# Kernel optimization log

Hardware: AMD Instinct MI355X
Metric: run time of the kernel (lower is better)

The kernel has to match this reference:

```python
import jax, jax.numpy as jnp
import numpy as np

B, TX, TY = 32, 64, 64
D, H, V = 512, 512, 32000
FORGET_BIAS = 1.0  # TF BasicLSTMCell default


def setup_inputs() -> dict:
    key = jax.random.key(0)
    ks = jax.random.split(key, 8)
    enc_ids = jax.random.randint(ks[0], (B, TX), 0, V, dtype=jnp.int32)
    dec_ids = jax.random.randint(ks[1], (B, TY), 0, V, dtype=jnp.int32)
    len_enc = jax.random.randint(ks[2], (B,), 1, TX + 1, dtype=jnp.int32)
    len_dec = jax.random.randint(ks[3], (B,), 1, TY + 1, dtype=jnp.int32)
    E = jax.random.normal(ks[4], (V, D), dtype=jnp.float32) * 0.05
    enc_W = jax.random.normal(ks[5], (D + H, 4 * H), dtype=jnp.float32) * (1.0 / np.sqrt(D + H))
    dec_W = jax.random.normal(ks[6], (D + H, 4 * H), dtype=jnp.float32) * (1.0 / np.sqrt(D + H))
    proj_W = jax.random.normal(ks[7], (H, V), dtype=jnp.float32) * (1.0 / np.sqrt(H))
    return {
        'encoder_inputs': enc_ids, 'decoder_inputs': dec_ids,
        'length_encoder': len_enc, 'length_decoder': len_dec,
        'E': E, 'enc_W': enc_W, 'enc_b': jnp.zeros((4 * H,), jnp.float32),
        'dec_W': dec_W, 'dec_b': jnp.zeros((4 * H,), jnp.float32),
        'proj_W': proj_W,
    }


def _lstm_scan(x_seq, lengths, W, b, c0, h0):
    """Masked LSTM over x_seq [T,B,D]; mimics tf.nn.dynamic_rnn sequence_length
    semantics (state frozen past each example's length). Returns (c,h,hs)."""
    def step(carry, x):
        c, h, t = carry
        z = jnp.concatenate([x, h], axis=-1) @ W + b  # [B,4H]
        i, j, f, o = jnp.split(z, 4, axis=-1)  # TF BasicLSTMCell gate order
        c_new = c * jax.nn.sigmoid(f + FORGET_BIAS) + jax.nn.sigmoid(i) * jnp.tanh(j)
        h_new = jnp.tanh(c_new) * jax.nn.sigmoid(o)
        m = (t < lengths)[:, None]
        c = jnp.where(m, c_new, c)
        h_out = jnp.where(m, h_new, jnp.zeros_like(h_new))  # emitted output zeroed past length
        h = jnp.where(m, h_new, h)
        return (c, h, t + 1), h_out
    (c, h, _), hs = jax.lax.scan(step, (c0, h0, jnp.int32(0)), x_seq)
    return c, h, hs


def reference(encoder_inputs, decoder_inputs, length_encoder, length_decoder,
              E, enc_W, enc_b, dec_W, dec_b, proj_W):
    b = encoder_inputs.shape[0]
    # Encoder: embed + masked LSTM; keep final state.
    enc_x = E[encoder_inputs].transpose(1, 0, 2)  # [TX,B,D]
    z = jnp.zeros((b, enc_W.shape[1] // 4), jnp.float32)
    c, h, _ = _lstm_scan(enc_x, length_encoder, enc_W, enc_b, z, z)
    # Decoder: teacher-forced LSTM from encoder final state + vocab projection.
    dec_x = E[decoder_inputs].transpose(1, 0, 2)  # [TY,B,D]
    _, _, hs = _lstm_scan(dec_x, length_decoder, dec_W, dec_b, c, h)  # [TY,B,H]
    logits = jnp.einsum('tbh,hv->btv', hs, proj_W)  # [B,TY,V]
    # impute_finished=True zeroes outputs past each sequence length
    mask = (jnp.arange(logits.shape[1])[None, :] < length_decoder[:, None])[:, :, None]
    return jnp.where(mask, logits, 0.0)
```

## Files before the change

### kernel.cpp

```cpp
#include <hip/hip_runtime.h>

typedef unsigned short ushort_t;
typedef __attribute__((ext_vector_type(8))) short short8;
typedef __attribute__((ext_vector_type(4))) float f32x4;

__device__ __forceinline__ ushort_t f2bf(float x) {
  union { float f; unsigned int u; } v; v.f = x;
  unsigned int r = v.u + 0x7fffu + ((v.u >> 16) & 1u);
  return (ushort_t)(r >> 16);
}
__device__ __forceinline__ float bf2f(ushort_t h) {
  union { unsigned int u; float f; } v; v.u = ((unsigned int)h) << 16; return v.f;
}
__device__ __forceinline__ void splitbf(float x, ushort_t& hi, ushort_t& lo) {
  hi = f2bf(x);
  lo = f2bf(x - bf2f(hi));
}
__device__ __forceinline__ float sigm(float x) { return 1.f / (1.f + expf(-x)); }
__device__ __forceinline__ f32x4 mfma16(short8 a, short8 b, f32x4 c) {
  return __builtin_amdgcn_mfma_f32_16x16x32_bf16(a, b, c, 0, 0, 0);
}

#define BAR_NB 64
__device__ __forceinline__ void gridbar(int* __restrict__ flags, int bid,
                                        int bm, int tid, int bar) {
  asm volatile("s_waitcnt vmcnt(0)" ::: "memory");
  __syncthreads();
  if (tid == 0)
    __hip_atomic_store(&flags[bid * 32], bar, __ATOMIC_RELAXED,
                       __HIP_MEMORY_SCOPE_AGENT);
  if (tid < 32) {
    while (__hip_atomic_load(&flags[(2 * tid + bm) * 32], __ATOMIC_RELAXED,
                             __HIP_MEMORY_SCOPE_AGENT) < bar) {}
  }
  __syncthreads();
}

__global__ void __launch_bounds__(256) transpose_split(
    const float* __restrict__ src, int ld, int k0,
    ushort_t* __restrict__ hi, ushort_t* __restrict__ lo) {
  __shared__ float tile[64][65];
  const int n0 = blockIdx.x * 64, kb = blockIdx.y * 64;
  #pragma unroll
  for (int i = 0; i < 16; ++i) {
    int idx = i * 256 + threadIdx.x;
    int kk = idx >> 6, nn = idx & 63;
    tile[kk][nn] = src[(size_t)(k0 + kb + kk) * ld + n0 + nn];
  }
  __syncthreads();
  #pragma unroll
  for (int i = 0; i < 16; ++i) {
    int idx = i * 256 + threadIdx.x;
    int nn = idx >> 6, kk = idx & 63;
    float x = tile[kk][nn];
    ushort_t h, l; splitbf(x, h, l);
    size_t o = (size_t)(n0 + nn) * 512 + kb + kk;
    hi[o] = h; lo[o] = l;
  }
}

__global__ void __launch_bounds__(128) embed_split(
    const int* __restrict__ ids, const float* __restrict__ E,
    ushort_t* __restrict__ Ahi, ushort_t* __restrict__ Alo, int T) {
  const int m = blockIdx.x;
  const int b = m & 31, t = m >> 5;
  const int id = ids[b * T + t];
  float4 v = ((const float4*)(E + (size_t)id * 512))[threadIdx.x];
  ushort_t h0, l0, h1, l1, h2, l2, h3, l3;
  splitbf(v.x, h0, l0); splitbf(v.y, h1, l1);
  splitbf(v.z, h2, l2); splitbf(v.w, h3, l3);
  ushort4 hv = make_ushort4(h0, h1, h2, h3);
  ushort4 lv = make_ushort4(l0, l1, l2, l3);
  ((ushort4*)(Ahi + (size_t)m * 512))[threadIdx.x] = hv;
  ((ushort4*)(Alo + (size_t)m * 512))[threadIdx.x] = lv;
}

template <int MFAST>
__global__ void __launch_bounds__(256, 2) gemm_split_t(
    const ushort_t* __restrict__ Ahi, const ushort_t* __restrict__ Alo,
    const ushort_t* __restrict__ Bhi, const ushort_t* __restrict__ Blo,
    const float* __restrict__ bias, float* __restrict__ C, int M, int N) {
  __shared__ __align__(16) ushort_t lAh[128 * 64];
  __shared__ __align__(16) ushort_t lAl[128 * 64];
  __shared__ __align__(16) ushort_t lBh[128 * 64];
  __shared__ __align__(16) ushort_t lBl[128 * 64];
  const int tid = threadIdx.x;
  const int lane = tid & 63, w = tid >> 6;
  const int wm = (w >> 1) * 64, wn = (w & 1) * 64;
  const int lm = lane & 15, lq = lane >> 4;
  const int m0 = (MFAST ? blockIdx.x : blockIdx.y) * 128;
  const int n0 = (MFAST ? blockIdx.y : blockIdx.x) * 128;

  f32x4 acc[4][4];
  #pragma unroll
  for (int i = 0; i < 4; ++i)
    #pragma unroll
    for (int j = 0; j < 4; ++j)
      acc[i][j] = (f32x4){0.f, 0.f, 0.f, 0.f};

  for (int kc = 0; kc < 8; ++kc) {
    if (kc) __syncthreads();
    #pragma unroll
    for (int i = 0; i < 4; ++i) {
      int cid = i * 256 + tid;
      int r = cid >> 3, c = cid & 7;
      int cs = c ^ (r & 7);
      size_t goffA = (size_t)(m0 + r) * 512 + kc * 64 + c * 8;
      size_t goffB = (size_t)(n0 + r) * 512 + kc * 64 + c * 8;
      *(uint4*)&lAh[r * 64 + cs * 8] = *(const uint4*)(Ahi + goffA);
      *(uint4*)&lAl[r * 64 + cs * 8] = *(const uint4*)(Alo + goffA);
      *(uint4*)&lBh[r * 64 + cs * 8] = *(const uint4*)(Bhi + goffB);
      *(uint4*)&lBl[r * 64 + cs * 8] = *(const uint4*)(Blo + goffB);
    }
    __syncthreads();
    #pragma unroll
    for (int ks = 0; ks < 2; ++ks) {
      short8 ah[4], al[4], bh[4], bl[4];
      #pragma unroll
      for (int t = 0; t < 4; ++t) {
        int ra = wm + t * 16 + lm;
        int ca = (ks * 4 + lq) ^ (ra & 7);
        ah[t] = *(const short8*)&lAh[ra * 64 + ca * 8];
        al[t] = *(const short8*)&lAl[ra * 64 + ca * 8];
        int rb = wn + t * 16 + lm;
        int cb = (ks * 4 + lq) ^ (rb & 7);
        bh[t] = *(const short8*)&lBh[rb * 64 + cb * 8];
        bl[t] = *(const short8*)&lBl[rb * 64 + cb * 8];
      }
      #pragma unroll
      for (int mt = 0; mt < 4; ++mt)
        #pragma unroll
        for (int nt = 0; nt < 4; ++nt) {
          acc[mt][nt] = mfma16(ah[mt], bh[nt], acc[mt][nt]);
          acc[mt][nt] = mfma16(ah[mt], bl[nt], acc[mt][nt]);
          acc[mt][nt] = mfma16(al[mt], bh[nt], acc[mt][nt]);
        }
    }
  }
  #pragma unroll
  for (int nt = 0; nt < 4; ++nt) {
    int col = n0 + wn + nt * 16 + lm;
    float bv = bias ? bias[col] : 0.f;
    #pragma unroll
    for (int mt = 0; mt < 4; ++mt) {
      int rbase = m0 + wm + mt * 16 + lq * 4;
      #pragma unroll
      for (int r = 0; r < 4; ++r)
        C[(size_t)(rbase + r) * N + col] = acc[mt][nt][r] + bv;
    }
  }
}

__global__ void __launch_bounds__(256, 1) lstm_recurrence(
    const ushort_t* __restrict__ eWh_hi, const ushort_t* __restrict__ eWh_lo,
    const ushort_t* __restrict__ dWh_hi, const ushort_t* __restrict__ dWh_lo,
    const float* __restrict__ xz_enc, const float* __restrict__ xz_dec,
    const int* __restrict__ len_enc, const int* __restrict__ len_dec,
    ushort_t* __restrict__ hseq_hi, ushort_t* __restrict__ hseq_lo,
    ushort_t* __restrict__ hs_hi, ushort_t* __restrict__ hs_lo,
    int* __restrict__ flags) {
  const int tid = threadIdx.x;
  const int lane = tid & 63, g = tid >> 6;
  const int lm = lane & 15, lq = lane >> 4;
  const int bm = blockIdx.x & 1, jg = blockIdx.x >> 1;

  __shared__ float z_x[4][16][17];
  __shared__ float c_st[16][17], h_st[16][17];

  const int bl = tid >> 4, nn = tid & 15;
  const int bglob = bm * 16 + bl;
  const int hcol = jg * 16 + nn;

  c_st[bl][nn] = 0.f; h_st[bl][nn] = 0.f;
  __hip_atomic_store(&hseq_hi[bglob * 512 + hcol], (ushort_t)0,
                     __ATOMIC_RELAXED, __HIP_MEMORY_SCOPE_AGENT);
  __hip_atomic_store(&hseq_lo[bglob * 512 + hcol], (ushort_t)0,
                     __ATOMIC_RELAXED, __HIP_MEMORY_SCOPE_AGENT);
  const int lenE = len_enc[bglob], lenD = len_dec[bglob];

  short8 fbh[16], fbl[16];
  const size_t browoff = (size_t)(g * 512 + jg * 16 + lm) * 512 + lq * 8;
  #pragma unroll
  for (int ks = 0; ks < 16; ++ks) {
    fbh[ks] = *(const short8*)(eWh_hi + browoff + ks * 32);
    fbl[ks] = *(const short8*)(eWh_lo + browoff + ks * 32);
  }

  float pzi, pzj, pzf, pzo;
  {
    const size_t base = (size_t)bglob * 2048 + jg * 16 + nn;
    pzi = xz_enc[base];        pzj = xz_enc[base + 512];
    pzf = xz_enc[base + 1024]; pzo = xz_enc[base + 1536];
  }
  gridbar(flags, blockIdx.x, bm, tid, 1);

  const size_t arow = (size_t)(bm * 16 + lm) * 512 + lq * 8;

  #pragma unroll 1
  for (int s = 0; s < 128; ++s) {
    if (s == 64) {
      #pragma unroll
      for (int ks = 0; ks < 16; ++ks) {
        fbh[ks] = *(const short8*)(dWh_hi + browoff + ks * 32);
        fbl[ks] = *(const short8*)(dWh_lo + browoff + ks * 32);
      }
    }
    const ushort_t* hh = hseq_hi + (size_t)s * 16384;
    const ushort_t* hl = hseq_lo + (size_t)s * 16384;
    ushort_t* ohh = hseq_hi + (size_t)(s + 1) * 16384;
    ushort_t* ohl = hseq_lo + (size_t)(s + 1) * 16384;

    f32x4 a0 = (f32x4){0.f, 0.f, 0.f, 0.f};
    f32x4 a1 = (f32x4){0.f, 0.f, 0.f, 0.f};
    f32x4 a2 = (f32x4){0.f, 0.f, 0.f, 0.f};
    #pragma unroll
    for (int ks = 0; ks < 16; ++ks) {
      short8 ah = *(const short8*)(hh + arow + ks * 32);
      short8 al = *(const short8*)(hl + arow + ks * 32);
      a0 = mfma16(ah, fbh[ks], a0);
      a1 = mfma16(ah, fbl[ks], a1);
      a2 = mfma16(al, fbh[ks], a2);
    }
    #pragma unroll
    for (int r = 0; r < 4; ++r)
      z_x[g][lq * 4 + r][lm] = a0[r] + a1[r] + a2[r];
    __syncthreads();

    {
      const bool isdec = s >= 64;
      const int t = isdec ? s - 64 : s;
      const int len = isdec ? lenD : lenE;
      float zi = z_x[0][bl][nn] + pzi;
      float zj = z_x[1][bl][nn] + pzj;
      float zf = z_x[2][bl][nn] + pzf;
      float zo = z_x[3][bl][nn] + pzo;
      float co = c_st[bl][nn], ho = h_st[bl][nn];
      float cn = co * sigm(zf + 1.0f) + sigm(zi) * tanhf(zj);
      float hn = tanhf(cn) * sigm(zo);
      bool msk = t < len;
      float ck = msk ? cn : co;
      float hk = msk ? hn : ho;
      c_st[bl][nn] = ck; h_st[bl][nn] = hk;
      ushort_t hi, lo;
      splitbf(hk, hi, lo);
      __hip_atomic_store(&ohh[bglob * 512 + hcol], hi, __ATOMIC_RELAXED,
                         __HIP_MEMORY_SCOPE_AGENT);
      __hip_atomic_store(&ohl[bglob * 512 + hcol], lo, __ATOMIC_RELAXED,
                         __HIP_MEMORY_SCOPE_AGENT);
      if (isdec) {
        float hv = msk ? hn : 0.f;
        splitbf(hv, hi, lo);
        hs_hi[((size_t)bglob * 64 + t) * 512 + hcol] = hi;
        hs_lo[((size_t)bglob * 64 + t) * 512 + hcol] = lo;
      }
    }
    if (s != 127) {
      asm volatile("s_waitcnt vmcnt(0)" ::: "memory");
      __syncthreads();
      if (tid == 0)
        __hip_atomic_store(&flags[blockIdx.x * 32], s + 2, __ATOMIC_RELAXED,
                           __HIP_MEMORY_SCOPE_AGENT);
      {
        const int sp = s + 1;
        const bool pd = sp >= 64;
        const float* xz = pd ? xz_dec : xz_enc;
        const int tp = pd ? sp - 64 : sp;
        const size_t base = ((size_t)tp * 32 + bglob) * 2048 + jg * 16 + nn;
        pzi = xz[base];        pzj = xz[base + 512];
        pzf = xz[base + 1024]; pzo = xz[base + 1536];
      }
      if (tid < 32) {
        while (__hip_atomic_load(&flags[(2 * tid + bm) * 32], __ATOMIC_RELAXED,
                                 __HIP_MEMORY_SCOPE_AGENT) < s + 2) {}
      }
      __syncthreads();
    }
  }
}

extern "C" void kernel_launch(void* const* d_in, const int* in_sizes, int n_in,
                              void* d_out, int out_size, void* d_ws, size_t ws_size,
                              hipStream_t stream) {
  (void)in_sizes; (void)n_in; (void)out_size; (void)ws_size;
  const int*   enc_ids = (const int*)d_in[0];
  const int*   dec_ids = (const int*)d_in[1];
  const int*   len_enc = (const int*)d_in[2];
  const int*   len_dec = (const int*)d_in[3];
  const float* E       = (const float*)d_in[4];
  const float* enc_W   = (const float*)d_in[5];
  const float* enc_b   = (const float*)d_in[6];
  const float* dec_W   = (const float*)d_in[7];
  const float* dec_b   = (const float*)d_in[8];
  const float* proj_W  = (const float*)d_in[9];

  char* w = (char*)d_ws;
  auto carve = [&](size_t bytes) -> char* {
    char* p = w; w += (bytes + 255) & ~(size_t)255; return p;
  };
  const size_t WSZ = 2048 * 512 * 2;
  ushort_t* eWx_hi = (ushort_t*)carve(WSZ); ushort_t* eWx_lo = (ushort_t*)carve(WSZ);
  ushort_t* eWh_hi = (ushort_t*)carve(WSZ); ushort_t* eWh_lo = (ushort_t*)carve(WSZ);
  ushort_t* dWx_hi = (ushort_t*)carve(WSZ); ushort_t* dWx_lo = (ushort_t*)carve(WSZ);
  ushort_t* dWh_hi = (ushort_t*)carve(WSZ); ushort_t* dWh_lo = (ushort_t*)carve(WSZ);
  ushort_t* pW_hi  = (ushort_t*)carve((size_t)32000 * 512 * 2);
  ushort_t* pW_lo  = (ushort_t*)carve((size_t)32000 * 512 * 2);
  ushort_t* Ae_hi  = (ushort_t*)carve(WSZ); ushort_t* Ae_lo = (ushort_t*)carve(WSZ);
  ushort_t* Ad_hi  = (ushort_t*)carve(WSZ); ushort_t* Ad_lo = (ushort_t*)carve(WSZ);
  float* xz_enc = (float*)carve((size_t)64 * 32 * 2048 * 4);
  float* xz_dec = (float*)carve((size_t)64 * 32 * 2048 * 4);
  ushort_t* hs_hi = (ushort_t*)carve(WSZ); ushort_t* hs_lo = (ushort_t*)carve(WSZ);
  ushort_t* hseq_hi = (ushort_t*)carve((size_t)129 * 32 * 512 * 2);
  ushort_t* hseq_lo = (ushort_t*)carve((size_t)129 * 32 * 512 * 2);
  int* flags = (int*)carve(BAR_NB * 32 * sizeof(int));

  dim3 blk(256);
  transpose_split<<<dim3(32, 8),  blk, 0, stream>>>(enc_W, 2048, 0,   eWx_hi, eWx_lo);
  transpose_split<<<dim3(32, 8),  blk, 0, stream>>>(enc_W, 2048, 512, eWh_hi, eWh_lo);
  transpose_split<<<dim3(32, 8),  blk, 0, stream>>>(dec_W, 2048, 0,   dWx_hi, dWx_lo);
  transpose_split<<<dim3(32, 8),  blk, 0, stream>>>(dec_W, 2048, 512, dWh_hi, dWh_lo);
  transpose_split<<<dim3(500, 8), blk, 0, stream>>>(proj_W, 32000, 0, pW_hi, pW_lo);

  embed_split<<<2048, 128, 0, stream>>>(enc_ids, E, Ae_hi, Ae_lo, 64);
  embed_split<<<2048, 128, 0, stream>>>(dec_ids, E, Ad_hi, Ad_lo, 64);

  gemm_split_t<0><<<dim3(16, 16), blk, 0, stream>>>(Ae_hi, Ae_lo, eWx_hi, eWx_lo,
                                                    enc_b, xz_enc, 2048, 2048);
  gemm_split_t<0><<<dim3(16, 16), blk, 0, stream>>>(Ad_hi, Ad_lo, dWx_hi, dWx_lo,
                                                    dec_b, xz_dec, 2048, 2048);

  void* args[] = { &eWh_hi, &eWh_lo, &dWh_hi, &dWh_lo,
                   (void*)&xz_enc, (void*)&xz_dec,
                   (void*)&len_enc, (void*)&len_dec,
                   &hseq_hi, &hseq_lo, &hs_hi, &hs_lo, &flags };
  hipLaunchCooperativeKernel((void*)lstm_recurrence, dim3(64), dim3(256),
                             args, 0, stream);

  const float* nobias = nullptr;
  gemm_split_t<1><<<dim3(16, 250), blk, 0, stream>>>(hs_hi, hs_lo, pW_hi, pW_lo,
                                                     nobias, (float*)d_out,
                                                     2048, 32000);
}
```

Measured before the change: 1.539 ms.

## Use direct global-to-LDS loads in projection GEMM and reorder barrier prefetch

Replaces register-staged tile copies in the projection GEMM with global_load_lds 16-byte direct-to-LDS loads, moving the XOR swizzle to the global source address. In the recurrent loop, the next-step xz prefetch now runs before a shared gridbar helper instead of overlapping the spin-wait. The direct loads cut VGPR traffic and instructions. The barrier change may expose the prefetch latency on every step, because gridbar waits for all outstanding loads before signalling.

New measurement: 1.514 ms. About the same (-1.6%).

```diff
diff --git a/kernel.cpp b/kernel.cpp
--- a/kernel.cpp
+++ b/kernel.cpp
@@ -19,6 +19,12 @@
 __device__ __forceinline__ float sigm(float x) { return 1.f / (1.f + expf(-x)); }
 __device__ __forceinline__ f32x4 mfma16(short8 a, short8 b, f32x4 c) {
   return __builtin_amdgcn_mfma_f32_16x16x32_bf16(a, b, c, 0, 0, 0);
+}
+
+__device__ __forceinline__ void gload16(const ushort_t* g, ushort_t* l) {
+  __builtin_amdgcn_global_load_lds(
+      (const __attribute__((address_space(1))) unsigned int*)g,
+      (__attribute__((address_space(3))) unsigned int*)l, 16, 0, 0);
 }
 
 #define BAR_NB 64
@@ -103,14 +109,15 @@
     #pragma unroll
     for (int i = 0; i < 4; ++i) {
       int cid = i * 256 + tid;
-      int r = cid >> 3, c = cid & 7;
-      int cs = c ^ (r & 7);
-      size_t goffA = (size_t)(m0 + r) * 512 + kc * 64 + c * 8;
-      size_t goffB = (size_t)(n0 + r) * 512 + kc * 64 + c * 8;
-      *(uint4*)&lAh[r * 64 + cs * 8] = *(const uint4*)(Ahi + goffA);
-      *(uint4*)&lAl[r * 64 + cs * 8] = *(const uint4*)(Alo + goffA);
-      *(uint4*)&lBh[r * 64 + cs * 8] = *(const uint4*)(Bhi + goffB);
-      *(uint4*)&lBl[r * 64 + cs * 8] = *(const uint4*)(Blo + goffB);
+      int r = cid >> 3, cl = cid & 7;
+      int csrc = cl ^ (r & 7);
+      size_t goffA = (size_t)(m0 + r) * 512 + kc * 64 + csrc * 8;
+      size_t goffB = (size_t)(n0 + r) * 512 + kc * 64 + csrc * 8;
+      int ldso = (i * 256 + w * 64) * 8;
+      gload16(Ahi + goffA, lAh + ldso);
+      gload16(Alo + goffA, lAl + ldso);
+      gload16(Bhi + goffB, lBh + ldso);
+      gload16(Blo + goffB, lBl + ldso);
     }
     __syncthreads();
     #pragma unroll
@@ -255,25 +262,14 @@
       }
     }
     if (s != 127) {
-      asm volatile("s_waitcnt vmcnt(0)" ::: "memory");
-      __syncthreads();
-      if (tid == 0)
-        __hip_atomic_store(&flags[blockIdx.x * 32], s + 2, __ATOMIC_RELAXED,
-                           __HIP_MEMORY_SCOPE_AGENT);
-      {
-        const int sp = s + 1;
-        const bool pd = sp >= 64;
-        const float* xz = pd ? xz_dec : xz_enc;
-        const int tp = pd ? sp - 64 : sp;
-        const size_t base = ((size_t)tp * 32 + bglob) * 2048 + jg * 16 + nn;
-        pzi = xz[base];        pzj = xz[base + 512];
-        pzf = xz[base + 1024]; pzo = xz[base + 1536];
-      }
-      if (tid < 32) {
-        while (__hip_atomic_load(&flags[(2 * tid + bm) * 32], __ATOMIC_RELAXED,
-                                 __HIP_MEMORY_SCOPE_AGENT) < s + 2) {}
-      }
-      __syncthreads();
+      const int sp = s + 1;
+      const bool pd = sp >= 64;
+      const float* xz = pd ? xz_dec : xz_enc;
+      const int tp = pd ? sp - 64 : sp;
+      const size_t base = ((size_t)tp * 32 + bglob) * 2048 + jg * 16 + nn;
+      pzi = xz[base];        pzj = xz[base + 512];
+      pzf = xz[base + 1024]; pzo = xz[base + 1536];
+      gridbar(flags, blockIdx.x, bm, tid, s + 2);
     }
   }
 }
```
